# Performance work log

Hardware: AMD Instinct MI355X
Metric: run time of the kernel (lower is better)

The kernel has to match this reference:

```python
import jax, jax.numpy as jnp
import numpy as np

BN_EPS = 1e-5
LN_EPS = 1e-5


def setup_inputs() -> dict:
    key = jax.random.key(0)
    ks = jax.random.split(key, 8)
    B, D, T = 16, 96, 512  # batch, enc_in (channels), d_model (time/feature)
    H = 2 * T
    residual = jax.random.normal(ks[0], (B, D, T), dtype=jnp.float32)
    # BatchNorm1d(enc_in) affine params
    bn_gamma = jnp.ones((D,), dtype=jnp.float32)
    bn_beta = jnp.zeros((D,), dtype=jnp.float32)
    # LayerNorm(d_model) affine params
    ln_gamma = jnp.ones((T,), dtype=jnp.float32)
    ln_beta = jnp.zeros((T,), dtype=jnp.float32)
    # MLP: Linear(T, 2T) -> GELU -> Linear(2T, T)
    W1 = jax.random.normal(ks[1], (T, H), dtype=jnp.float32) / np.float32(np.sqrt(T))
    b1 = jnp.zeros((H,), dtype=jnp.float32)
    W2 = jax.random.normal(ks[2], (H, T), dtype=jnp.float32) / np.float32(np.sqrt(H))
    b2 = jnp.zeros((T,), dtype=jnp.float32)
    return {"residual": residual, "bn_gamma": bn_gamma, "bn_beta": bn_beta,
            "ln_gamma": ln_gamma, "ln_beta": ln_beta,
            "W1": W1, "b1": b1, "W2": W2, "b2": b2}


def _var_cor_attention(x):
    # x: [B, D, T]; queries = keys = values = x
    B, D, T = x.shape
    f = jnp.fft.rfft(x, axis=-1)                       # [B, D, F]
    # pairwise spectral product q_i * conj(k_j): [B, D, D, F]
    res = f[:, :, None, :] * jnp.conj(f[:, None, :, :])
    corr = jnp.fft.irfft(res, axis=-1).mean(axis=-1)   # [B, D, D]
    scale = np.float32(1.0 / np.sqrt(T))
    corr = jax.nn.softmax(corr * scale, axis=-1)
    V = jnp.einsum('bsd,bde->bse', corr, x)            # [B, D, T]
    return V


def reference(residual, bn_gamma, bn_beta, ln_gamma, ln_beta, W1, b1, W2, b2):
    # attention + residual
    x = _var_cor_attention(residual) + residual        # [B, D, T]
    # BatchNorm1d over channel dim D: stats over (B, T), biased variance
    mu = x.mean(axis=(0, 2), keepdims=True)
    var = ((x - mu) ** 2).mean(axis=(0, 2), keepdims=True)
    x = (x - mu) * jax.lax.rsqrt(var + BN_EPS)
    x = x * bn_gamma[None, :, None] + bn_beta[None, :, None]
    # MLP (exact GELU, torch default) + residual
    h = jax.nn.gelu(jnp.einsum('bdt,th->bdh', x, W1) + b1, approximate=False)
    y = jnp.einsum('bdh,ht->bdt', h, W2) + b2 + x
    # LayerNorm over last dim T
    mu2 = y.mean(axis=-1, keepdims=True)
    var2 = ((y - mu2) ** 2).mean(axis=-1, keepdims=True)
    y = (y - mu2) * jax.lax.rsqrt(var2 + LN_EPS)
    return y * ln_gamma + ln_beta
```

## Files before the change

### kernel.cpp

```cpp
#include <hip/hip_runtime.h>
#include <math.h>
#include <stdint.h>

#define BB 16
#define DD 96
#define TT 512
#define HH 1024
#define NROW (BB*DD)
#define KT2 (HH/32)

typedef __attribute__((ext_vector_type(4))) float floatx4;
typedef __attribute__((ext_vector_type(8))) short short8;

#define WSOFF_X     0u
#define WSOFF_A     3145728u
#define WSOFF_HFRAG WSOFF_A
#define WSOFF_W1BF  6291456u
#define WSOFF_W2BF  7340032u
#define WSOFF_PS    8388608u
#define WSOFF_PS2   8437760u
#define WSOFF_SCSH  8486912u

__device__ __forceinline__ uint16_t f2bf(float v) {
    uint32_t u = __float_as_uint(v);
    uint32_t r = 0x7fffu + ((u >> 16) & 1u);
    return (uint16_t)((u + r) >> 16);
}

__global__ __launch_bounds__(256) void k_pre(const float* __restrict__ residual,
                                             const float* __restrict__ W1,
                                             const float* __restrict__ W2,
                                             float* __restrict__ A,
                                             uint16_t* __restrict__ w1bf,
                                             uint16_t* __restrict__ w2bf) {
    __shared__ float sl[DD];
    const int bid = blockIdx.x;
    const int tid = threadIdx.x;
    const int wave = tid >> 6;
    const int lane = tid & 63;
    const int q = lane >> 4, l15 = lane & 15;

    if (bid < BB) {
        #pragma unroll
        for (int rr = 0; rr < 24; ++rr) {
            int i = wave*24 + rr;
            const float* p = residual + ((size_t)bid*DD + i)*TT;
            float acc = 0.f;
            #pragma unroll
            for (int u = 0; u < TT/64; ++u) acc += p[lane + u*64];
            #pragma unroll
            for (int o = 32; o > 0; o >>= 1) acc += __shfl_down(acc, o, 64);
            if (lane == 0) sl[i] = acc;
        }
        __syncthreads();
        if (tid < DD) {
            const float c = 1.0f / (512.0f * 22.627416997969522f);
            float si = sl[tid] * c;
            float m = -1e30f;
            for (int j = 0; j < DD; ++j) m = fmaxf(m, si * sl[j]);
            float sum = 0.f;
            for (int j = 0; j < DD; ++j) sum += __expf(si * sl[j] - m);
            float inv = 1.0f / sum;
            float* Ao = A + ((size_t)bid*DD + tid)*DD;
            for (int j = 0; j < DD; ++j) Ao[j] = __expf(si * sl[j] - m) * inv;
        }
    } else {
        int wgid = (bid - BB)*4 + wave;
        const int nw = (512 - BB)*4;
        for (int u = wgid; u < 2048; u += nw) {
            const float* W; uint16_t* ob; int KT, N, b;
            if (u < 1024) { W = W1; ob = w1bf; KT = 16; N = 1024; b = u; }
            else          { W = W2; ob = w2bf; KT = 32; N = 512;  b = u - 1024; }
            int tile_n = b / KT, tile_k = b % KT;
            const float* src = W + (size_t)(tile_k*32 + q*8)*N + tile_n*16 + l15;
            uint16_t tmp[8];
            #pragma unroll
            for (int j = 0; j < 8; ++j) tmp[j] = f2bf(src[(size_t)j*N]);
            uint16_t* dst = ob + ((size_t)b*64 + lane)*8;
            *reinterpret_cast<ushort4*>(dst)     = *reinterpret_cast<ushort4*>(&tmp[0]);
            *reinterpret_cast<ushort4*>(dst + 4) = *reinterpret_cast<ushort4*>(&tmp[4]);
        }
    }
}

__global__ __launch_bounds__(256) void k_attn(const float* __restrict__ residual,
                                              const float* __restrict__ A,
                                              float* __restrict__ x,
                                              float* __restrict__ ps,
                                              float* __restrict__ ps2) {
    __shared__ float rlds[DD*64];
    const int u = blockIdx.x;
    const int b = u >> 5, chunk = (u >> 2) & 7, ig = u & 3;
    const int tid = threadIdx.x;
    const int wave = tid >> 6;
    const int lane = tid & 63;

    const float4* rb4 = reinterpret_cast<const float4*>(residual + (size_t)b*DD*TT);
    float4* rl4 = reinterpret_cast<float4*>(rlds);
    #pragma unroll
    for (int s = 0; s < 6; ++s) {
        int idx = tid + s*256;
        int i = idx >> 4, t4 = idx & 15;
        rl4[idx] = rb4[(size_t)i*(TT/4) + chunk*16 + t4];
    }
    __syncthreads();

    int i0 = ig*24 + wave*6;
    const float* Ab = A + ((size_t)b*DD + i0)*DD;
    float acc[6];
    #pragma unroll
    for (int rr = 0; rr < 6; ++rr) acc[rr] = rlds[(i0+rr)*64 + lane];
    #pragma unroll 4
    for (int j4 = 0; j4 < DD/4; ++j4) {
        float4 a[6];
        #pragma unroll
        for (int rr = 0; rr < 6; ++rr)
            a[rr] = *reinterpret_cast<const float4*>(Ab + rr*DD + j4*4);
        float rv[4];
        #pragma unroll
        for (int uu = 0; uu < 4; ++uu) rv[uu] = rlds[(j4*4+uu)*64 + lane];
        #pragma unroll
        for (int rr = 0; rr < 6; ++rr) {
            acc[rr] = fmaf(a[rr].x, rv[0], acc[rr]);
            acc[rr] = fmaf(a[rr].y, rv[1], acc[rr]);
            acc[rr] = fmaf(a[rr].z, rv[2], acc[rr]);
            acc[rr] = fmaf(a[rr].w, rv[3], acc[rr]);
        }
    }
    #pragma unroll
    for (int rr = 0; rr < 6; ++rr) {
        float v = acc[rr];
        x[((size_t)b*DD + i0 + rr)*TT + chunk*64 + lane] = v;
        float s1 = v, s2 = v*v;
        #pragma unroll
        for (int o = 32; o > 0; o >>= 1) {
            s1 += __shfl_down(s1, o, 64);
            s2 += __shfl_down(s2, o, 64);
        }
        if (lane == 0) {
            int d = i0 + rr;
            ps [d*128 + b*8 + chunk] = s1;
            ps2[d*128 + b*8 + chunk] = s2;
        }
    }
}

__global__ __launch_bounds__(256) void k_gemm1(const float* __restrict__ x,
                                               const float* __restrict__ ps,
                                               const float* __restrict__ ps2,
                                               const float* __restrict__ bng,
                                               const float* __restrict__ bnb,
                                               const uint16_t* __restrict__ w1bf,
                                               const float* __restrict__ b1,
                                               uint16_t* __restrict__ hfrag,
                                               float* __restrict__ scsh) {
    __shared__ __align__(16) char SM[27136];
    uint16_t* fragA = (uint16_t*)SM;
    uint16_t* cs    = (uint16_t*)(SM + 16384);
    float*    fin   = (float*)(SM + 24832);
    float*    scs   = (float*)(SM + 26368);
    const int bid = blockIdx.x;
    const int tid = threadIdx.x;
    const int wave = tid >> 6;
    const int lane = tid & 63;
    const int q = lane >> 4, l15 = lane & 15;

    if (tid < 192) {
        int d = tid >> 1, h = tid & 1;
        const float4* p1 = reinterpret_cast<const float4*>(ps  + d*128 + h*64);
        const float4* p2 = reinterpret_cast<const float4*>(ps2 + d*128 + h*64);
        float a1 = 0.f, a2 = 0.f;
        #pragma unroll
        for (int j = 0; j < 16; ++j) {
            float4 v = p1[j]; a1 += v.x+v.y+v.z+v.w;
            float4 w = p2[j]; a2 += w.x+w.y+w.z+w.w;
        }
        fin[tid*2]   = a1;
        fin[tid*2+1] = a2;
    }
    __syncthreads();
    if (tid < DD) {
        float s1 = fin[tid*4]   + fin[tid*4+2];
        float s2 = fin[tid*4+1] + fin[tid*4+3];
        const float invn = 1.0f / (float)(BB*TT);
        float mu  = s1 * invn;
        float var = s2 * invn - mu*mu;
        float rs  = rsqrtf(var + 1e-5f);
        float scv = rs * bng[tid];
        float shv = bnb[tid] - mu*scv;
        scs[tid]      = scv;
        scs[DD + tid] = shv;
        if (bid == 0) { scsh[tid] = scv; scsh[DD + tid] = shv; }
    }
    __syncthreads();

    const int mtile = bid >> 2, nq = bid & 3;
    #pragma unroll
    for (int r4 = 0; r4 < 4; ++r4) {
        int pi = tid + r4*256;
        int kk = pi >> 6, pl = pi & 63;
        int pq = pl >> 4, pr = pl & 15;
        int row = mtile*16 + pr;
        int d = row % DD;
        float scv = scs[d], shv = scs[DD + d];
        const float* xp = x + (size_t)row*TT + kk*32 + pq*8;
        float4 v0 = *reinterpret_cast<const float4*>(xp);
        float4 v1 = *reinterpret_cast<const float4*>(xp + 4);
        ushort4 o0, o1;
        o0.x = f2bf(v0.x*scv + shv); o0.y = f2bf(v0.y*scv + shv);
        o0.z = f2bf(v0.z*scv + shv); o0.w = f2bf(v0.w*scv + shv);
        o1.x = f2bf(v1.x*scv + shv); o1.y = f2bf(v1.y*scv + shv);
        o1.z = f2bf(v1.z*scv + shv); o1.w = f2bf(v1.w*scv + shv);
        uint16_t* fp = fragA + ((size_t)kk*64 + pl)*8;
        *reinterpret_cast<ushort4*>(fp)     = o0;
        *reinterpret_cast<ushort4*>(fp + 4) = o1;
    }
    __syncthreads();

    int n0 = nq*256 + wave*64;
    floatx4 acc4[4] = {};
    #pragma unroll
    for (int kk = 0; kk < 16; ++kk) {
        short8 a = *reinterpret_cast<const short8*>(fragA + (kk*64 + lane)*8);
        #pragma unroll
        for (int nf = 0; nf < 4; ++nf) {
            int ct = (n0 >> 4) + nf;
            short8 bfr = *reinterpret_cast<const short8*>(
                w1bf + ((size_t)(ct*16 + kk)*64 + lane)*8);
            acc4[nf] = __builtin_amdgcn_mfma_f32_16x16x32_bf16(a, bfr, acc4[nf], 0, 0, 0);
        }
    }
    #pragma unroll
    for (int nf = 0; nf < 4; ++nf) {
        int coll = wave*64 + nf*16 + l15;
        float bias = b1[nq*256 + coll];
        #pragma unroll
        for (int r = 0; r < 4; ++r) {
            float v = acc4[nf][r] + bias;
            float gl = 0.5f * v * (1.0f + erff(v * 0.7071067811865475f));
            cs[(q*4 + r)*264 + coll] = f2bf(gl);
        }
    }
    __syncthreads();
    #pragma unroll
    for (int cc = 0; cc < 2; ++cc) {
        int c = wave*2 + cc;
        const uint4* srcp = reinterpret_cast<const uint4*>(cs + l15*264 + c*32 + q*8);
        size_t chunk = (size_t)mtile*KT2 + nq*8 + c;
        reinterpret_cast<uint4*>(hfrag)[chunk*64 + lane] = *srcp;
    }
}

__global__ __launch_bounds__(256) void k_gemm2(const uint16_t* __restrict__ hfrag,
                                               const uint16_t* __restrict__ w2bf,
                                               const float* __restrict__ b2,
                                               const float* __restrict__ x,
                                               const float* __restrict__ scsh,
                                               const float* __restrict__ lng,
                                               const float* __restrict__ lnb,
                                               float* __restrict__ out) {
    __shared__ float lnred[128];
    const int mtile = blockIdx.x;
    const int tid = threadIdx.x;
    const int wave = tid >> 6;
    const int lane = tid & 63;
    const int q = lane >> 4, l15 = lane & 15;
    const int m0 = mtile*16;
    const int n0 = wave*128;

    floatx4 acc[8] = {};
    const uint16_t* ap = hfrag + ((size_t)mtile*KT2*64 + lane)*8;
    #pragma unroll
    for (int kk = 0; kk < 32; ++kk) {
        short8 a = *reinterpret_cast<const short8*>(ap + kk*512);
        #pragma unroll
        for (int nf = 0; nf < 8; ++nf) {
            int ct = (n0 >> 4) + nf;
            short8 bfr = *reinterpret_cast<const short8*>(
                w2bf + ((size_t)(ct*32 + kk)*64 + lane)*8);
            acc[nf] = __builtin_amdgcn_mfma_f32_16x16x32_bf16(a, bfr, acc[nf], 0, 0, 0);
        }
    }
    float s_pt[4]  = {0.f,0.f,0.f,0.f};
    float s2_pt[4] = {0.f,0.f,0.f,0.f};
    #pragma unroll
    for (int r = 0; r < 4; ++r) {
        int row = m0 + q*4 + r;
        int d = row % DD;
        float scv = scsh[d], shv = scsh[DD + d];
        #pragma unroll
        for (int nf = 0; nf < 8; ++nf) {
            int col = n0 + nf*16 + l15;
            float v = acc[nf][r] + b2[col] + x[(size_t)row*TT + col]*scv + shv;
            acc[nf][r] = v;
            s_pt[r]  += v;
            s2_pt[r] += v*v;
        }
    }
    #pragma unroll
    for (int o = 1; o < 16; o <<= 1) {
        #pragma unroll
        for (int r = 0; r < 4; ++r) {
            s_pt[r]  += __shfl_xor(s_pt[r],  o, 64);
            s2_pt[r] += __shfl_xor(s2_pt[r], o, 64);
        }
    }
    if (l15 == 0) {
        #pragma unroll
        for (int r = 0; r < 4; ++r) {
            lnred[(wave*16 + q*4 + r)*2]     = s_pt[r];
            lnred[(wave*16 + q*4 + r)*2 + 1] = s2_pt[r];
        }
    }
    __syncthreads();
    #pragma unroll
    for (int r = 0; r < 4; ++r) {
        int rloc = q*4 + r;
        float s1 = lnred[rloc*2]   + lnred[(16+rloc)*2]   + lnred[(32+rloc)*2]   + lnred[(48+rloc)*2];
        float s2 = lnred[rloc*2+1] + lnred[(16+rloc)*2+1] + lnred[(32+rloc)*2+1] + lnred[(48+rloc)*2+1];
        const float invT = 1.0f / (float)TT;
        float mu  = s1 * invT;
        float var = s2 * invT - mu*mu;
        float rs  = rsqrtf(var + 1e-5f);
        int row = m0 + rloc;
        #pragma unroll
        for (int nf = 0; nf < 8; ++nf) {
            int col = n0 + nf*16 + l15;
            out[(size_t)row*TT + col] = (acc[nf][r] - mu)*rs*lng[col] + lnb[col];
        }
    }
}

extern "C" void kernel_launch(void* const* d_in, const int* in_sizes, int n_in,
                              void* d_out, int out_size, void* d_ws, size_t ws_size,
                              hipStream_t stream) {
    (void)in_sizes; (void)n_in; (void)out_size; (void)ws_size;
    const float* residual = (const float*)d_in[0];
    const float* bng = (const float*)d_in[1];
    const float* bnb = (const float*)d_in[2];
    const float* lng = (const float*)d_in[3];
    const float* lnb = (const float*)d_in[4];
    const float* W1  = (const float*)d_in[5];
    const float* b1  = (const float*)d_in[6];
    const float* W2  = (const float*)d_in[7];
    const float* b2  = (const float*)d_in[8];
    float* out = (float*)d_out;
    char* ws = (char*)d_ws;
    float*    x     = (float*)(ws + WSOFF_X);
    float*    A     = (float*)(ws + WSOFF_A);
    uint16_t* hfrag = (uint16_t*)(ws + WSOFF_HFRAG);
    uint16_t* w1bf  = (uint16_t*)(ws + WSOFF_W1BF);
    uint16_t* w2bf  = (uint16_t*)(ws + WSOFF_W2BF);
    float*    ps    = (float*)(ws + WSOFF_PS);
    float*    ps2   = (float*)(ws + WSOFF_PS2);
    float*    scsh  = (float*)(ws + WSOFF_SCSH);

    k_pre  <<<512, 256, 0, stream>>>(residual, W1, W2, A, w1bf, w2bf);
    k_attn <<<512, 256, 0, stream>>>(residual, A, x, ps, ps2);
    k_gemm1<<<384, 256, 0, stream>>>(x, ps, ps2, bng, bnb, w1bf, b1, hfrag, scsh);
    k_gemm2<<<96, 256, 0, stream>>>(hfrag, w2bf, b2, x, scsh, lng, lnb, out);
}
```

Baseline: 134.0 us.

## Recompute softmax in attention, regrid GEMMs, split LayerNorm into own kernel

The row-sum reduction in k_pre is spread over 96 blocks instead of 16. The softmax matrix is now computed per block in LDS inside k_attn rather than written to global memory and reread. Both GEMM kernels use 2D grids with narrower N tiles per wave, which gives more blocks, and each block computes only its own 16 rows of BatchNorm scale/shift. LayerNorm moves out of the k_gemm2 epilogue into a separate k_ln kernel. That adds a launch and an extra read and write of the output in exchange for more parallelism in GEMM2.

```diff
diff --git a/kernel.cpp b/kernel.cpp
--- a/kernel.cpp
+++ b/kernel.cpp
@@ -13,13 +13,12 @@
 typedef __attribute__((ext_vector_type(8))) short short8;
 
 #define WSOFF_X     0u
-#define WSOFF_A     3145728u
-#define WSOFF_HFRAG WSOFF_A
+#define WSOFF_HFRAG 3145728u
 #define WSOFF_W1BF  6291456u
 #define WSOFF_W2BF  7340032u
 #define WSOFF_PS    8388608u
 #define WSOFF_PS2   8437760u
-#define WSOFF_SCSH  8486912u
+#define WSOFF_S     8486912u
 
 __device__ __forceinline__ uint16_t f2bf(float v) {
     uint32_t u = __float_as_uint(v);
@@ -30,43 +29,36 @@
 __global__ __launch_bounds__(256) void k_pre(const float* __restrict__ residual,
                                              const float* __restrict__ W1,
                                              const float* __restrict__ W2,
-                                             float* __restrict__ A,
+                                             float* __restrict__ s,
                                              uint16_t* __restrict__ w1bf,
                                              uint16_t* __restrict__ w2bf) {
-    __shared__ float sl[DD];
     const int bid = blockIdx.x;
     const int tid = threadIdx.x;
     const int wave = tid >> 6;
     const int lane = tid & 63;
     const int q = lane >> 4, l15 = lane & 15;
 
-    if (bid < BB) {
-        #pragma unroll
-        for (int rr = 0; rr < 24; ++rr) {
-            int i = wave*24 + rr;
-            const float* p = residual + ((size_t)bid*DD + i)*TT;
-            float acc = 0.f;
+    if (bid < 96) {
+        int row0 = bid*16 + wave*4;
+        float acc[4] = {0.f, 0.f, 0.f, 0.f};
+        #pragma unroll
+        for (int cc = 0; cc < 4; ++cc) {
+            const float* p = residual + (size_t)(row0 + cc)*TT;
             #pragma unroll
-            for (int u = 0; u < TT/64; ++u) acc += p[lane + u*64];
+            for (int u = 0; u < TT/64; ++u) acc[cc] += p[lane + u*64];
+        }
+        #pragma unroll
+        for (int o = 32; o > 0; o >>= 1) {
             #pragma unroll
-            for (int o = 32; o > 0; o >>= 1) acc += __shfl_down(acc, o, 64);
-            if (lane == 0) sl[i] = acc;
-        }
-        __syncthreads();
-        if (tid < DD) {
-            const float c = 1.0f / (512.0f * 22.627416997969522f);
-            float si = sl[tid] * c;
-            float m = -1e30f;
-            for (int j = 0; j < DD; ++j) m = fmaxf(m, si * sl[j]);
-            float sum = 0.f;
-            for (int j = 0; j < DD; ++j) sum += __expf(si * sl[j] - m);
-            float inv = 1.0f / sum;
-            float* Ao = A + ((size_t)bid*DD + tid)*DD;
-            for (int j = 0; j < DD; ++j) Ao[j] = __expf(si * sl[j] - m) * inv;
+            for (int cc = 0; cc < 4; ++cc) acc[cc] += __shfl_down(acc[cc], o, 64);
+        }
+        if (lane == 0) {
+            #pragma unroll
+            for (int cc = 0; cc < 4; ++cc) s[row0 + cc] = acc[cc];
         }
     } else {
-        int wgid = (bid - BB)*4 + wave;
-        const int nw = (512 - BB)*4;
+        int wgid = (bid - 96)*4 + wave;
+        const int nw = (512 - 96)*4;
         for (int u = wgid; u < 2048; u += nw) {
             const float* W; uint16_t* ob; int KT, N, b;
             if (u < 1024) { W = W1; ob = w1bf; KT = 16; N = 1024; b = u; }
@@ -84,11 +76,13 @@
 }
 
 __global__ __launch_bounds__(256) void k_attn(const float* __restrict__ residual,
-                                              const float* __restrict__ A,
+                                              const float* __restrict__ s,
                                               float* __restrict__ x,
                                               float* __restrict__ ps,
                                               float* __restrict__ ps2) {
     __shared__ float rlds[DD*64];
+    __shared__ float slds[DD];
+    __shared__ float aLDS[24*DD];
     const int u = blockIdx.x;
     const int b = u >> 5, chunk = (u >> 2) & 7, ig = u & 3;
     const int tid = threadIdx.x;
@@ -98,15 +92,37 @@
     const float4* rb4 = reinterpret_cast<const float4*>(residual + (size_t)b*DD*TT);
     float4* rl4 = reinterpret_cast<float4*>(rlds);
     #pragma unroll
-    for (int s = 0; s < 6; ++s) {
-        int idx = tid + s*256;
+    for (int sx = 0; sx < 6; ++sx) {
+        int idx = tid + sx*256;
         int i = idx >> 4, t4 = idx & 15;
         rl4[idx] = rb4[(size_t)i*(TT/4) + chunk*16 + t4];
     }
-    __syncthreads();
+    if (tid < DD) slds[tid] = s[b*DD + tid];
+    __syncthreads();
+
+    const float c = 1.0f / (512.0f * 22.627416997969522f);
+    float sj_lo = slds[lane];
+    float sj_hi = (lane < 32) ? slds[64 + lane] : 0.f;
+    #pragma unroll
+    for (int rr = 0; rr < 6; ++rr) {
+        int iloc = wave*6 + rr;
+        float si = slds[ig*24 + iloc] * c;
+        float v1 = si * sj_lo;
+        float v2 = (lane < 32) ? si * sj_hi : -1e30f;
+        float m = fmaxf(v1, v2);
+        #pragma unroll
+        for (int o = 1; o < 64; o <<= 1) m = fmaxf(m, __shfl_xor(m, o, 64));
+        float p1 = __expf(v1 - m);
+        float p2 = (lane < 32) ? __expf(v2 - m) : 0.f;
+        float sum = p1 + p2;
+        #pragma unroll
+        for (int o = 1; o < 64; o <<= 1) sum += __shfl_xor(sum, o, 64);
+        float inv = 1.0f / sum;
+        aLDS[iloc*DD + lane] = p1 * inv;
+        if (lane < 32) aLDS[iloc*DD + 64 + lane] = p2 * inv;
+    }
 
     int i0 = ig*24 + wave*6;
-    const float* Ab = A + ((size_t)b*DD + i0)*DD;
     float acc[6];
     #pragma unroll
     for (int rr = 0; rr < 6; ++rr) acc[rr] = rlds[(i0+rr)*64 + lane];
@@ -115,7 +131,7 @@
         float4 a[6];
         #pragma unroll
         for (int rr = 0; rr < 6; ++rr)
-            a[rr] = *reinterpret_cast<const float4*>(Ab + rr*DD + j4*4);
+            a[rr] = *reinterpret_cast<const float4*>(&aLDS[(wave*6+rr)*DD + j4*4]);
         float rv[4];
         #pragma unroll
         for (int uu = 0; uu < 4; ++uu) rv[uu] = rlds[(j4*4+uu)*64 + lane];
@@ -141,6 +157,37 @@
             int d = i0 + rr;
             ps [d*128 + b*8 + chunk] = s1;
             ps2[d*128 + b*8 + chunk] = s2;
+        }
+    }
+}
+
+__device__ __forceinline__ void bn_finalize16(const float* __restrict__ ps,
+                                              const float* __restrict__ ps2,
+                                              const float* __restrict__ bng,
+                                              const float* __restrict__ bnb,
+                                              int m0, int tid, float* scs) {
+    if (tid < 256) {
+        int dg = tid >> 4, uu = tid & 15;
+        int d = (m0 + dg) % DD;
+        const float4* p1 = reinterpret_cast<const float4*>(ps  + d*128 + uu*8);
+        const float4* p2 = reinterpret_cast<const float4*>(ps2 + d*128 + uu*8);
+        float4 a0 = p1[0], a1 = p1[1];
+        float4 b0 = p2[0], b1 = p2[1];
+        float s1 = a0.x+a0.y+a0.z+a0.w + a1.x+a1.y+a1.z+a1.w;
+        float s2 = b0.x+b0.y+b0.z+b0.w + b1.x+b1.y+b1.z+b1.w;
+        #pragma unroll
+        for (int o = 1; o < 16; o <<= 1) {
+            s1 += __shfl_xor(s1, o, 16);
+            s2 += __shfl_xor(s2, o, 16);
+        }
+        if (uu == 0) {
+            const float invn = 1.0f / (float)(BB*TT);
+            float mu  = s1 * invn;
+            float var = s2 * invn - mu*mu;
+            float rs  = rsqrtf(var + 1e-5f);
+            float scv = rs * bng[d];
+            scs[dg*2]     = scv;
+            scs[dg*2 + 1] = bnb[d] - mu*scv;
         }
     }
 }
@@ -152,58 +199,27 @@
                                                const float* __restrict__ bnb,
                                                const uint16_t* __restrict__ w1bf,
                                                const float* __restrict__ b1,
-                                               uint16_t* __restrict__ hfrag,
-                                               float* __restrict__ scsh) {
-    __shared__ __align__(16) char SM[27136];
-    uint16_t* fragA = (uint16_t*)SM;
-    uint16_t* cs    = (uint16_t*)(SM + 16384);
-    float*    fin   = (float*)(SM + 24832);
-    float*    scs   = (float*)(SM + 26368);
-    const int bid = blockIdx.x;
+                                               uint16_t* __restrict__ hfrag) {
+    __shared__ __align__(16) uint16_t fragA[16*64*8];
+    __shared__ __align__(16) uint16_t cs[16][136];
+    __shared__ float scs[32];
+    const int mtile = blockIdx.x;
+    const int m0 = mtile*16;
     const int tid = threadIdx.x;
     const int wave = tid >> 6;
     const int lane = tid & 63;
     const int q = lane >> 4, l15 = lane & 15;
 
-    if (tid < 192) {
-        int d = tid >> 1, h = tid & 1;
-        const float4* p1 = reinterpret_cast<const float4*>(ps  + d*128 + h*64);
-        const float4* p2 = reinterpret_cast<const float4*>(ps2 + d*128 + h*64);
-        float a1 = 0.f, a2 = 0.f;
-        #pragma unroll
-        for (int j = 0; j < 16; ++j) {
-            float4 v = p1[j]; a1 += v.x+v.y+v.z+v.w;
-            float4 w = p2[j]; a2 += w.x+w.y+w.z+w.w;
-        }
-        fin[tid*2]   = a1;
-        fin[tid*2+1] = a2;
-    }
-    __syncthreads();
-    if (tid < DD) {
-        float s1 = fin[tid*4]   + fin[tid*4+2];
-        float s2 = fin[tid*4+1] + fin[tid*4+3];
-        const float invn = 1.0f / (float)(BB*TT);
-        float mu  = s1 * invn;
-        float var = s2 * invn - mu*mu;
-        float rs  = rsqrtf(var + 1e-5f);
-        float scv = rs * bng[tid];
-        float shv = bnb[tid] - mu*scv;
-        scs[tid]      = scv;
-        scs[DD + tid] = shv;
-        if (bid == 0) { scsh[tid] = scv; scsh[DD + tid] = shv; }
-    }
-    __syncthreads();
-
-    const int mtile = bid >> 2, nq = bid & 3;
+    bn_finalize16(ps, ps2, bng, bnb, m0, tid, scs);
+    __syncthreads();
+
     #pragma unroll
     for (int r4 = 0; r4 < 4; ++r4) {
         int pi = tid + r4*256;
         int kk = pi >> 6, pl = pi & 63;
         int pq = pl >> 4, pr = pl & 15;
-        int row = mtile*16 + pr;
-        int d = row % DD;
-        float scv = scs[d], shv = scs[DD + d];
-        const float* xp = x + (size_t)row*TT + kk*32 + pq*8;
+        float scv = scs[pr*2], shv = scs[pr*2 + 1];
+        const float* xp = x + (size_t)(m0 + pr)*TT + kk*32 + pq*8;
         float4 v0 = *reinterpret_cast<const float4*>(xp);
         float4 v1 = *reinterpret_cast<const float4*>(xp + 4);
         ushort4 o0, o1;
@@ -217,36 +233,34 @@
     }
     __syncthreads();
 
-    int n0 = nq*256 + wave*64;
-    floatx4 acc4[4] = {};
+    const int n0 = blockIdx.y*128 + wave*32;
+    floatx4 acc4[2] = {};
+    const uint16_t* b0p = w1bf + ((size_t)((n0>>4)    )*16*64 + lane)*8;
+    const uint16_t* b1p = w1bf + ((size_t)((n0>>4) + 1)*16*64 + lane)*8;
     #pragma unroll
     for (int kk = 0; kk < 16; ++kk) {
-        short8 a = *reinterpret_cast<const short8*>(fragA + (kk*64 + lane)*8);
-        #pragma unroll
-        for (int nf = 0; nf < 4; ++nf) {
-            int ct = (n0 >> 4) + nf;
-            short8 bfr = *reinterpret_cast<const short8*>(
-                w1bf + ((size_t)(ct*16 + kk)*64 + lane)*8);
-            acc4[nf] = __builtin_amdgcn_mfma_f32_16x16x32_bf16(a, bfr, acc4[nf], 0, 0, 0);
-        }
-    }
-    #pragma unroll
-    for (int nf = 0; nf < 4; ++nf) {
-        int coll = wave*64 + nf*16 + l15;
-        float bias = b1[nq*256 + coll];
+        short8 a  = *reinterpret_cast<const short8*>(fragA + (kk*64 + lane)*8);
+        short8 bb0 = *reinterpret_cast<const short8*>(b0p + kk*512);
+        short8 bb1 = *reinterpret_cast<const short8*>(b1p + kk*512);
+        acc4[0] = __builtin_amdgcn_mfma_f32_16x16x32_bf16(a, bb0, acc4[0], 0, 0, 0);
+        acc4[1] = __builtin_amdgcn_mfma_f32_16x16x32_bf16(a, bb1, acc4[1], 0, 0, 0);
+    }
+    #pragma unroll
+    for (int nf = 0; nf < 2; ++nf) {
+        int coll = wave*32 + nf*16 + l15;
+        float bias = b1[blockIdx.y*128 + coll];
         #pragma unroll
         for (int r = 0; r < 4; ++r) {
             float v = acc4[nf][r] + bias;
             float gl = 0.5f * v * (1.0f + erff(v * 0.7071067811865475f));
-            cs[(q*4 + r)*264 + coll] = f2bf(gl);
-        }
-    }
-    __syncthreads();
-    #pragma unroll
-    for (int cc = 0; cc < 2; ++cc) {
-        int c = wave*2 + cc;
-        const uint4* srcp = reinterpret_cast<const uint4*>(cs + l15*264 + c*32 + q*8);
-        size_t chunk = (size_t)mtile*KT2 + nq*8 + c;
+            cs[q*4 + r][coll] = f2bf(gl);
+        }
+    }
+    __syncthreads();
+    {
+        int cchunk = wave;
+        const uint4* srcp = reinterpret_cast<const uint4*>(&cs[l15][cchunk*32 + q*8]);
+        size_t chunk = (size_t)mtile*KT2 + (blockIdx.y*4 + cchunk);
         reinterpret_cast<uint4*>(hfrag)[chunk*64 + lane] = *srcp;
     }
 }
@@ -255,80 +269,77 @@
                                                const uint16_t* __restrict__ w2bf,
                                                const float* __restrict__ b2,
                                                const float* __restrict__ x,
-                                               const float* __restrict__ scsh,
-                                               const float* __restrict__ lng,
-                                               const float* __restrict__ lnb,
-                                               float* __restrict__ out) {
-    __shared__ float lnred[128];
+                                               const float* __restrict__ ps,
+                                               const float* __restrict__ ps2,
+                                               const float* __restrict__ bng,
+                                               const float* __restrict__ bnb,
+                                               float* __restrict__ y) {
+    __shared__ float scs[32];
     const int mtile = blockIdx.x;
+    const int m0 = mtile*16;
     const int tid = threadIdx.x;
     const int wave = tid >> 6;
     const int lane = tid & 63;
     const int q = lane >> 4, l15 = lane & 15;
-    const int m0 = mtile*16;
-    const int n0 = wave*128;
-
-    floatx4 acc[8] = {};
-    const uint16_t* ap = hfrag + ((size_t)mtile*KT2*64 + lane)*8;
+    const int n0 = blockIdx.y*128 + wave*32;
+
+    bn_finalize16(ps, ps2, bng, bnb, m0, tid, scs);
+    __syncthreads();
+
+    floatx4 acc[2] = {};
+    const uint16_t* ap  = hfrag + ((size_t)mtile*KT2*64 + lane)*8;
+    const uint16_t* b0p = w2bf + ((size_t)((n0>>4)    )*32*64 + lane)*8;
+    const uint16_t* b1p = w2bf + ((size_t)((n0>>4) + 1)*32*64 + lane)*8;
     #pragma unroll
     for (int kk = 0; kk < 32; ++kk) {
-        short8 a = *reinterpret_cast<const short8*>(ap + kk*512);
-        #pragma unroll
-        for (int nf = 0; nf < 8; ++nf) {
-            int ct = (n0 >> 4) + nf;
-            short8 bfr = *reinterpret_cast<const short8*>(
-                w2bf + ((size_t)(ct*32 + kk)*64 + lane)*8);
-            acc[nf] = __builtin_amdgcn_mfma_f32_16x16x32_bf16(a, bfr, acc[nf], 0, 0, 0);
-        }
-    }
-    float s_pt[4]  = {0.f,0.f,0.f,0.f};
-    float s2_pt[4] = {0.f,0.f,0.f,0.f};
-    #pragma unroll
-    for (int r = 0; r < 4; ++r) {
-        int row = m0 + q*4 + r;
-        int d = row % DD;
-        float scv = scsh[d], shv = scsh[DD + d];
-        #pragma unroll
-        for (int nf = 0; nf < 8; ++nf) {
-            int col = n0 + nf*16 + l15;
-            float v = acc[nf][r] + b2[col] + x[(size_t)row*TT + col]*scv + shv;
-            acc[nf][r] = v;
-            s_pt[r]  += v;
-            s2_pt[r] += v*v;
-        }
-    }
-    #pragma unroll
-    for (int o = 1; o < 16; o <<= 1) {
+        short8 a  = *reinterpret_cast<const short8*>(ap  + kk*512);
+        short8 bb0 = *reinterpret_cast<const short8*>(b0p + kk*512);
+        short8 bb1 = *reinterpret_cast<const short8*>(b1p + kk*512);
+        acc[0] = __builtin_amdgcn_mfma_f32_16x16x32_bf16(a, bb0, acc[0], 0, 0, 0);
+        acc[1] = __builtin_amdgcn_mfma_f32_16x16x32_bf16(a, bb1, acc[1], 0, 0, 0);
+    }
+    #pragma unroll
+    for (int nf = 0; nf < 2; ++nf) {
+        int col = n0 + nf*16 + l15;
+        float bias = b2[col];
         #pragma unroll
         for (int r = 0; r < 4; ++r) {
-            s_pt[r]  += __shfl_xor(s_pt[r],  o, 64);
-            s2_pt[r] += __shfl_xor(s2_pt[r], o, 64);
-        }
-    }
-    if (l15 == 0) {
-        #pragma unroll
-        for (int r = 0; r < 4; ++r) {
-            lnred[(wave*16 + q*4 + r)*2]     = s_pt[r];
-            lnred[(wave*16 + q*4 + r)*2 + 1] = s2_pt[r];
-        }
-    }
-    __syncthreads();
-    #pragma unroll
-    for (int r = 0; r < 4; ++r) {
-        int rloc = q*4 + r;
-        float s1 = lnred[rloc*2]   + lnred[(16+rloc)*2]   + lnred[(32+rloc)*2]   + lnred[(48+rloc)*2];
-        float s2 = lnred[rloc*2+1] + lnred[(16+rloc)*2+1] + lnred[(32+rloc)*2+1] + lnred[(48+rloc)*2+1];
-        const float invT = 1.0f / (float)TT;
-        float mu  = s1 * invT;
-        float var = s2 * invT - mu*mu;
-        float rs  = rsqrtf(var + 1e-5f);
-        int row = m0 + rloc;
-        #pragma unroll
-        for (int nf = 0; nf < 8; ++nf) {
-            int col = n0 + nf*16 + l15;
-            out[(size_t)row*TT + col] = (acc[nf][r] - mu)*rs*lng[col] + lnb[col];
-        }
-    }
+            int rloc = q*4 + r;
+            int row = m0 + rloc;
+            float xb = x[(size_t)row*TT + col]*scs[rloc*2] + scs[rloc*2 + 1];
+            y[(size_t)row*TT + col] = acc[nf][r] + bias + xb;
+        }
+    }
+}
+
+__global__ __launch_bounds__(64) void k_ln(float* __restrict__ y,
+                                           const float* __restrict__ lng,
+                                           const float* __restrict__ lnb) {
+    int row = blockIdx.x;
+    int lane = threadIdx.x;
+    float4* p = reinterpret_cast<float4*>(y + (size_t)row*TT);
+    float4 v0 = p[lane*2], v1 = p[lane*2 + 1];
+    float s  = v0.x+v0.y+v0.z+v0.w + v1.x+v1.y+v1.z+v1.w;
+    float s2 = v0.x*v0.x+v0.y*v0.y+v0.z*v0.z+v0.w*v0.w
+             + v1.x*v1.x+v1.y*v1.y+v1.z*v1.z+v1.w*v1.w;
+    #pragma unroll
+    for (int o = 1; o < 64; o <<= 1) {
+        s  += __shfl_xor(s,  o, 64);
+        s2 += __shfl_xor(s2, o, 64);
+    }
+    float mu = s * (1.0f/TT);
+    float var = s2 * (1.0f/TT) - mu*mu;
+    float rs = rsqrtf(var + 1e-5f);
+    const float4* g4 = reinterpret_cast<const float4*>(lng);
+    const float4* b4 = reinterpret_cast<const float4*>(lnb);
+    float4 g0 = g4[lane*2], g1 = g4[lane*2+1];
+    float4 bb0 = b4[lane*2], bb1 = b4[lane*2+1];
+    float4 o0, o1;
+    o0.x = (v0.x-mu)*rs*g0.x + bb0.x;  o0.y = (v0.y-mu)*rs*g0.y + bb0.y;
+    o0.z = (v0.z-mu)*rs*g0.z + bb0.z;  o0.w = (v0.w-mu)*rs*g0.w + bb0.w;
+    o1.x = (v1.x-mu)*rs*g1.x + bb1.x;  o1.y = (v1.y-mu)*rs*g1.y + bb1.y;
+    o1.z = (v1.z-mu)*rs*g1.z + bb1.z;  o1.w = (v1.w-mu)*rs*g1.w + bb1.w;
+    p[lane*2] = o0;  p[lane*2+1] = o1;
 }
 
 extern "C" void kernel_launch(void* const* d_in, const int* in_sizes, int n_in,
@@ -347,16 +358,16 @@
     float* out = (float*)d_out;
     char* ws = (char*)d_ws;
     float*    x     = (float*)(ws + WSOFF_X);
-    float*    A     = (float*)(ws + WSOFF_A);
     uint16_t* hfrag = (uint16_t*)(ws + WSOFF_HFRAG);
     uint16_t* w1bf  = (uint16_t*)(ws + WSOFF_W1BF);
     uint16_t* w2bf  = (uint16_t*)(ws + WSOFF_W2BF);
     float*    ps    = (float*)(ws + WSOFF_PS);
     float*    ps2   = (float*)(ws + WSOFF_PS2);
-    float*    scsh  = (float*)(ws + WSOFF_SCSH);
-
-    k_pre  <<<512, 256, 0, stream>>>(residual, W1, W2, A, w1bf, w2bf);
-    k_attn <<<512, 256, 0, stream>>>(residual, A, x, ps, ps2);
-    k_gemm1<<<384, 256, 0, stream>>>(x, ps, ps2, bng, bnb, w1bf, b1, hfrag, scsh);
-    k_gemm2<<<96, 256, 0, stream>>>(hfrag, w2bf, b2, x, scsh, lng, lnb, out);
-}
+    float*    s     = (float*)(ws + WSOFF_S);
+
+    k_pre  <<<512, 256, 0, stream>>>(residual, W1, W2, s, w1bf, w2bf);
+    k_attn <<<512, 256, 0, stream>>>(residual, s, x, ps, ps2);
+    k_gemm1<<<dim3(96, 8), 256, 0, stream>>>(x, ps, ps2, bng, bnb, w1bf, b1, hfrag);
+    k_gemm2<<<dim3(96, 4), 256, 0, stream>>>(hfrag, w2bf, b2, x, ps, ps2, bng, bnb, out);
+    k_ln   <<<NROW, 64, 0, stream>>>(out, lng, lnb);
+}
```

Result: faster. 112.1 us (-16.4%).
